# Optimization experiments

Measured on AMD Instinct MI355X. Metric: run time of the kernel, lower is better.

The kernel has to match this reference:

```python
import jax, jax.numpy as jnp
import numpy as np

# Mamba2 defaults (mamba_ssm): expand=2, headdim=64, d_conv=4, ngroups=1
D_MODEL, D_STATE, D_INNER, HEADDIM, D_CONV = 512, 64, 1024, 64, 4
NHEADS = D_INNER // HEADDIM  # 16
CONV_DIM = D_INNER + 2 * D_STATE  # 1152
D_IN_PROJ = 2 * D_INNER + 2 * D_STATE + NHEADS  # 2192
BATCH, SEQLEN = 2, 2048
RMS_EPS = 1.1920929e-07  # torch nn.RMSNorm eps=None -> fp32 machine eps
GNORM_EPS = 1e-5  # mamba_ssm RMSNormGated default


def _rms(t, w, eps):
    return t * jax.lax.rsqrt(jnp.mean(t * t, axis=-1, keepdims=True) + eps) * w


def _mamba2(u, in_w, conv_w, conv_b, dt_bias, A_log, Dp, gnorm_w, out_w):
    """Mamba2 block forward (ngroups=1). u: (b, l, d_model) -> (b, l, d_model)."""
    b, l, _ = u.shape
    zxbcdt = jnp.einsum('bld,ed->ble', u, in_w)  # (b, l, 2192)
    z = zxbcdt[..., :D_INNER]
    xBC = zxbcdt[..., D_INNER:D_INNER + CONV_DIM]
    dt = jax.nn.softplus(zxbcdt[..., -NHEADS:] + dt_bias)  # (b, l, h)
    # causal depthwise conv, kernel D_CONV, then SiLU
    xp = jnp.pad(xBC, ((0, 0), (D_CONV - 1, 0), (0, 0)))
    xBC = conv_b + sum(xp[:, i:i + l, :] * conv_w[:, i] for i in range(D_CONV))
    xBC = jax.nn.silu(xBC)
    x = xBC[..., :D_INNER].reshape(b, l, NHEADS, HEADDIM)
    Bm = xBC[..., D_INNER:D_INNER + D_STATE]  # (b, l, n)
    Cm = xBC[..., D_INNER + D_STATE:]         # (b, l, n)
    dA = jnp.exp(dt * (-jnp.exp(A_log)))      # (b, l, h), decay per head

    def step(h, inp):
        dA_t, dt_t, B_t, C_t, x_t = inp  # (b,h) (b,h) (b,n) (b,n) (b,h,p)
        h = h * dA_t[:, :, None, None] + jnp.einsum('bh,bhp,bn->bhpn', dt_t, x_t, B_t)
        y = jnp.einsum('bhpn,bn->bhp', h, C_t)
        return h, y

    h0 = jnp.zeros((b, NHEADS, HEADDIM, D_STATE), u.dtype)
    xs = (jnp.swapaxes(dA, 0, 1), jnp.swapaxes(dt, 0, 1), jnp.swapaxes(Bm, 0, 1),
          jnp.swapaxes(Cm, 0, 1), jnp.swapaxes(x, 0, 1))
    _, ys = jax.lax.scan(step, h0, xs)  # (l, b, h, p)
    y = jnp.swapaxes(ys, 0, 1) + x * Dp[None, None, :, None]
    y = y.reshape(b, l, D_INNER)
    # gated RMSNorm: norm(y * silu(z)) * weight
    y = y * jax.nn.silu(z)
    y = _rms(y, gnorm_w, GNORM_EPS)
    return jnp.einsum('bli,oi->blo', y, out_w)


def _layer(x, pos_emb, pixel_mask, norm_ssm_w, norm_ffn_w, ffn_w1, ffn_b1, ffn_w2, ffn_b2,
           f_in_w, f_conv_w, f_conv_b, f_dt_bias, f_A_log, f_D, f_gnorm_w, f_out_w,
           b_in_w, b_conv_w, b_conv_b, b_dt_bias, b_A_log, b_D, b_gnorm_w, b_out_w):
    si = _rms(x, norm_ssm_w, RMS_EPS) + pos_emb
    fwd = _mamba2(si, f_in_w, f_conv_w, f_conv_b, f_dt_bias, f_A_log, f_D, f_gnorm_w, f_out_w)
    bwd = jnp.flip(_mamba2(jnp.flip(si, 1), b_in_w, b_conv_w, b_conv_b, b_dt_bias,
                           b_A_log, b_D, b_gnorm_w, b_out_w), 1)
    ssm_out = (fwd + bwd) * pixel_mask[..., None]  # merge='add'
    x = x + ssm_out
    h = _rms(x, norm_ffn_w, RMS_EPS)
    h = jax.nn.gelu(h @ ffn_w1.T + ffn_b1, approximate=False)
    return x + (h @ ffn_w2.T + ffn_b2)


def setup_inputs() -> dict:
    key = jax.random.key(0)
    ks = jax.random.split(key, 16)
    f32 = jnp.float32
    inp = {}
    inp['x'] = jax.random.normal(ks[0], (BATCH, SEQLEN, D_MODEL), f32)
    inp['pos_emb'] = jax.random.normal(ks[1], (BATCH, SEQLEN, D_MODEL), f32) * 0.02
    inp['pixel_mask'] = jnp.ones((BATCH, SEQLEN), f32)
    inp['norm_ssm_w'] = jnp.ones((D_MODEL,), f32)
    inp['norm_ffn_w'] = jnp.ones((D_MODEL,), f32)
    d_ffn = 4 * D_MODEL
    inp['ffn_w1'] = jax.random.normal(ks[2], (d_ffn, D_MODEL), f32) * 0.02
    inp['ffn_b1'] = jnp.zeros((d_ffn,), f32)
    inp['ffn_w2'] = jax.random.normal(ks[3], (D_MODEL, d_ffn), f32) * 0.02
    inp['ffn_b2'] = jnp.zeros((D_MODEL,), f32)
    i = 4
    for pre in ('f', 'b'):
        inp[pre + '_in_w'] = jax.random.normal(ks[i], (D_IN_PROJ, D_MODEL), f32) * 0.02; i += 1
        inp[pre + '_conv_w'] = jax.random.uniform(ks[i], (CONV_DIM, D_CONV), f32, -0.5, 0.5); i += 1
        inp[pre + '_conv_b'] = jnp.zeros((CONV_DIM,), f32)
        dt0 = jnp.exp(jax.random.uniform(ks[i], (NHEADS,), f32) * (jnp.log(0.1) - jnp.log(0.001)) + jnp.log(0.001)); i += 1
        inp[pre + '_dt_bias'] = dt0 + jnp.log(-jnp.expm1(-dt0))  # inverse softplus
        inp[pre + '_A_log'] = jnp.log(jax.random.uniform(ks[i], (NHEADS,), f32, 1.0, 16.0)); i += 1
        inp[pre + '_D'] = jnp.ones((NHEADS,), f32)
        inp[pre + '_gnorm_w'] = jnp.ones((D_INNER,), f32)
        inp[pre + '_out_w'] = jax.random.normal(ks[i], (D_MODEL, D_INNER), f32) * 0.02; i += 1
    return inp


def reference(x, pos_emb, pixel_mask, norm_ssm_w, norm_ffn_w, ffn_w1, ffn_b1, ffn_w2, ffn_b2,
              f_in_w, f_conv_w, f_conv_b, f_dt_bias, f_A_log, f_D, f_gnorm_w, f_out_w,
              b_in_w, b_conv_w, b_conv_b, b_dt_bias, b_A_log, b_D, b_gnorm_w, b_out_w):
    return _layer(x, pos_emb, pixel_mask, norm_ssm_w, norm_ffn_w, ffn_w1, ffn_b1, ffn_w2, ffn_b2,
                  f_in_w, f_conv_w, f_conv_b, f_dt_bias, f_A_log, f_D, f_gnorm_w, f_out_w,
                  b_in_w, b_conv_w, b_conv_b, b_dt_bias, b_A_log, b_D, b_gnorm_w, b_out_w)
```

## Files before the change

### kernel.cpp

```cpp
#include <hip/hip_runtime.h>
#include <hip/hip_bf16.h>

typedef unsigned short u16;
typedef unsigned int u32;
typedef __bf16 bf16x8 __attribute__((ext_vector_type(8)));
typedef float f32x4 __attribute__((ext_vector_type(4)));

typedef __attribute__((address_space(1))) void gvoid_t;
typedef __attribute__((address_space(3))) void lvoid_t;
__device__ __forceinline__ void lds_cp16(void* lds, const void* g) {
    __builtin_amdgcn_global_load_lds((gvoid_t*)g, (lvoid_t*)lds, 16, 0, 0);
}

__device__ __forceinline__ float bf2f(u16 v) {
    u32 x = (u32)v << 16;
    return __builtin_bit_cast(float, x);
}
__device__ __forceinline__ u16 f2bf(float f) {
    return __builtin_bit_cast(u16, (__bf16)f);
}

__device__ __forceinline__ float block_sum_256(float v, float* red) {
    #pragma unroll
    for (int o = 32; o > 0; o >>= 1) v += __shfl_xor(v, o);
    int w = threadIdx.x >> 6;
    if ((threadIdx.x & 63) == 0) red[w] = v;
    __syncthreads();
    return red[0] + red[1] + red[2] + red[3];
}

__global__ __launch_bounds__(256) void k_prep(
    const float* __restrict__ f_inw, const float* __restrict__ b_inw,
    const float* __restrict__ f_ow, const float* __restrict__ b_ow,
    const float* __restrict__ w1, const float* __restrict__ w2,
    u16* __restrict__ INWF, u16* __restrict__ INWB,
    u16* __restrict__ OWF, u16* __restrict__ OWB,
    u16* __restrict__ W1B, u16* __restrict__ W2B,
    const float* __restrict__ x, const float* __restrict__ pe,
    const float* __restrict__ wrms, u16* __restrict__ sib) {
    if (blockIdx.x < 21504) {
        int i = blockIdx.x * 256 + threadIdx.x;
        if (i < 1179648) { int n = i >> 9; INWF[i] = (n < 2192) ? f2bf(f_inw[i]) : (u16)0; return; }
        i -= 1179648;
        if (i < 1179648) { int n = i >> 9; INWB[i] = (n < 2192) ? f2bf(b_inw[i]) : (u16)0; return; }
        i -= 1179648;
        if (i < 524288) { OWF[i] = f2bf(f_ow[i]); return; }
        i -= 524288;
        if (i < 524288) { OWB[i] = f2bf(b_ow[i]); return; }
        i -= 524288;
        if (i < 1048576) { W1B[i] = f2bf(w1[i]); return; }
        i -= 1048576;
        if (i < 1048576) W2B[i] = f2bf(w2[i]);
        return;
    }
    __shared__ float red[4];
    int row = blockIdx.x - 21504, t = threadIdx.x;
    size_t base = (size_t)row * 512 + t * 2;
    float2 xv = *(const float2*)(x + base);
    float ss = block_sum_256(xv.x * xv.x + xv.y * xv.y, red);
    float sc = rsqrtf(ss * (1.f / 512.f) + 1.1920929e-07f);
    float2 pv = *(const float2*)(pe + base);
    float2 wv = *(const float2*)(wrms + t * 2);
    sib[base] = f2bf(xv.x * sc * wv.x + pv.x);
    sib[base + 1] = f2bf(xv.y * sc * wv.y + pv.y);
}

__global__ __launch_bounds__(256) void k_gemm_in(
    const u16* __restrict__ A, const u16* __restrict__ W0, const u16* __restrict__ W1,
    u16* __restrict__ Z0, u16* __restrict__ Z1,
    u16* __restrict__ XB0, u16* __restrict__ XB1) {
    const int z = blockIdx.z;
    const u16* W = z ? W1 : W0;
    u16* Z = z ? Z1 : Z0;
    u16* XB = z ? XB1 : XB0;
    const int K = 512;

    __shared__ __align__(16) u16 As[128 * 32];
    __shared__ __align__(16) u16 Bs[128 * 32];

    const int t = threadIdx.x;
    const int lane = t & 63;
    const int w = t >> 6;
    const int m0 = blockIdx.y * 128;
    const int n0 = blockIdx.x * 128;
    const int wm = (w >> 1) * 64;
    const int wn = (w & 1) * 64;
    const int fr = lane & 15;
    const int fk = (lane >> 4) * 8;

    f32x4 acc[4][4];
    #pragma unroll
    for (int i = 0; i < 4; ++i)
        #pragma unroll
        for (int j = 0; j < 4; ++j) acc[i][j] = (f32x4){0.f, 0.f, 0.f, 0.f};

    for (int kt = 0; kt < K; kt += 32) {
        #pragma unroll
        for (int j = 0; j < 2; ++j) {
            int off16 = j * 256 + t;
            int row = off16 >> 2;
            int kc = (off16 & 3) * 8;
            int gm = m0 + row;
            if (z) gm = (gm & ~2047) | (2047 - (gm & 2047));
            lds_cp16(As + off16 * 8, A + (size_t)gm * K + kt + kc);
            lds_cp16(Bs + off16 * 8, W + (size_t)(n0 + row) * K + kt + kc);
        }
        __syncthreads();
        bf16x8 af[4], bfr[4];
        #pragma unroll
        for (int i = 0; i < 4; ++i) af[i] = *(const bf16x8*)(As + (wm + i * 16 + fr) * 32 + fk);
        #pragma unroll
        for (int i = 0; i < 4; ++i) bfr[i] = *(const bf16x8*)(Bs + (wn + i * 16 + fr) * 32 + fk);
        #pragma unroll
        for (int i = 0; i < 4; ++i)
            #pragma unroll
            for (int j = 0; j < 4; ++j)
                acc[i][j] = __builtin_amdgcn_mfma_f32_16x16x32_bf16(af[i], bfr[j], acc[i][j], 0, 0, 0);
        __syncthreads();
    }
    #pragma unroll
    for (int i = 0; i < 4; ++i) {
        int rbase = m0 + wm + i * 16 + (lane >> 4) * 4;
        #pragma unroll
        for (int j = 0; j < 4; ++j) {
            int c = n0 + wn + j * 16 + fr;
            #pragma unroll
            for (int r = 0; r < 4; ++r) {
                u16 v = f2bf(acc[i][j][r]);
                int m = rbase + r;
                if (c < 1024) Z[(size_t)m * 1024 + c] = v;
                else if (c < 2192) XB[(size_t)m * 1184 + (c - 1024)] = v;
            }
        }
    }
}

template <int EPI>
__global__ __launch_bounds__(256) void k_gemm128(
    const u16* __restrict__ A0, const u16* __restrict__ A1,
    const u16* __restrict__ W0, const u16* __restrict__ W1,
    u16* __restrict__ C0, u16* __restrict__ C1, int N, int K,
    const float* __restrict__ bias, const float* __restrict__ resid,
    float* __restrict__ outf) {
    const int z = blockIdx.z;
    const u16* A = z ? A1 : A0;
    const u16* W = z ? W1 : W0;
    u16* C = z ? C1 : C0;

    __shared__ __align__(16) u16 As[128 * 32];
    __shared__ __align__(16) u16 Bs[128 * 32];

    const int t = threadIdx.x;
    const int lane = t & 63;
    const int w = t >> 6;
    const int m0 = blockIdx.y * 128;
    const int n0 = blockIdx.x * 128;
    const int wm = (w >> 1) * 64;
    const int wn = (w & 1) * 64;
    const int fr = lane & 15;
    const int fk = (lane >> 4) * 8;

    f32x4 acc[4][4];
    #pragma unroll
    for (int i = 0; i < 4; ++i)
        #pragma unroll
        for (int j = 0; j < 4; ++j) acc[i][j] = (f32x4){0.f, 0.f, 0.f, 0.f};

    for (int kt = 0; kt < K; kt += 32) {
        #pragma unroll
        for (int j = 0; j < 2; ++j) {
            int off16 = j * 256 + t;
            int row = off16 >> 2;
            int kc = (off16 & 3) * 8;
            lds_cp16(As + off16 * 8, A + (size_t)(m0 + row) * K + kt + kc);
            lds_cp16(Bs + off16 * 8, W + (size_t)(n0 + row) * K + kt + kc);
        }
        __syncthreads();
        bf16x8 af[4], bfr[4];
        #pragma unroll
        for (int i = 0; i < 4; ++i) af[i] = *(const bf16x8*)(As + (wm + i * 16 + fr) * 32 + fk);
        #pragma unroll
        for (int i = 0; i < 4; ++i) bfr[i] = *(const bf16x8*)(Bs + (wn + i * 16 + fr) * 32 + fk);
        #pragma unroll
        for (int i = 0; i < 4; ++i)
            #pragma unroll
            for (int j = 0; j < 4; ++j)
                acc[i][j] = __builtin_amdgcn_mfma_f32_16x16x32_bf16(af[i], bfr[j], acc[i][j], 0, 0, 0);
        __syncthreads();
    }
    #pragma unroll
    for (int i = 0; i < 4; ++i) {
        int rbase = m0 + wm + i * 16 + (lane >> 4) * 4;
        #pragma unroll
        for (int j = 0; j < 4; ++j) {
            int col = n0 + wn + j * 16 + fr;
            #pragma unroll
            for (int r = 0; r < 4; ++r) {
                int m = rbase + r;
                float v = acc[i][j][r];
                if (EPI == 0) {
                    C[(size_t)m * N + col] = f2bf(v);
                } else if (EPI == 1) {
                    float xg = v + bias[col];
                    C[(size_t)m * N + col] = f2bf(0.5f * xg * (1.f + erff(xg * 0.70710678118654752f)));
                } else {
                    outf[(size_t)m * N + col] = v + bias[col] + resid[(size_t)m * N + col];
                }
            }
        }
    }
}

template <int EPI>
__global__ __launch_bounds__(256) void k_gemm12864(
    const u16* __restrict__ A0, const u16* __restrict__ A1,
    const u16* __restrict__ W0, const u16* __restrict__ W1,
    u16* __restrict__ C0, u16* __restrict__ C1, int N, int K,
    const float* __restrict__ bias, const float* __restrict__ resid,
    float* __restrict__ outf) {
    const int z = blockIdx.z;
    const u16* A = z ? A1 : A0;
    const u16* W = z ? W1 : W0;
    u16* C = z ? C1 : C0;

    __shared__ __align__(16) u16 As[128 * 32];
    __shared__ __align__(16) u16 Bs[64 * 32];

    const int t = threadIdx.x;
    const int lane = t & 63;
    const int w = t >> 6;
    const int m0 = blockIdx.y * 128;
    const int n0 = blockIdx.x * 64;
    const int wm = w * 32;
    const int fr = lane & 15;
    const int fk = (lane >> 4) * 8;

    f32x4 acc[2][4];
    #pragma unroll
    for (int i = 0; i < 2; ++i)
        #pragma unroll
        for (int j = 0; j < 4; ++j) acc[i][j] = (f32x4){0.f, 0.f, 0.f, 0.f};

    for (int kt = 0; kt < K; kt += 32) {
        #pragma unroll
        for (int j = 0; j < 2; ++j) {
            int off16 = j * 256 + t;
            int row = off16 >> 2;
            int kc = (off16 & 3) * 8;
            lds_cp16(As + off16 * 8, A + (size_t)(m0 + row) * K + kt + kc);
        }
        lds_cp16(Bs + t * 8, W + (size_t)(n0 + (t >> 2)) * K + kt + (t & 3) * 8);
        __syncthreads();
        bf16x8 af[2], bfr[4];
        #pragma unroll
        for (int i = 0; i < 2; ++i) af[i] = *(const bf16x8*)(As + (wm + i * 16 + fr) * 32 + fk);
        #pragma unroll
        for (int j = 0; j < 4; ++j) bfr[j] = *(const bf16x8*)(Bs + (j * 16 + fr) * 32 + fk);
        #pragma unroll
        for (int i = 0; i < 2; ++i)
            #pragma unroll
            for (int j = 0; j < 4; ++j)
                acc[i][j] = __builtin_amdgcn_mfma_f32_16x16x32_bf16(af[i], bfr[j], acc[i][j], 0, 0, 0);
        __syncthreads();
    }
    #pragma unroll
    for (int i = 0; i < 2; ++i) {
        int rbase = m0 + wm + i * 16 + (lane >> 4) * 4;
        #pragma unroll
        for (int j = 0; j < 4; ++j) {
            int col = n0 + j * 16 + fr;
            #pragma unroll
            for (int r = 0; r < 4; ++r) {
                int m = rbase + r;
                float v = acc[i][j][r];
                if (EPI == 0) {
                    C[(size_t)m * N + col] = f2bf(v);
                } else if (EPI == 1) {
                    float xg = v + bias[col];
                    C[(size_t)m * N + col] = f2bf(0.5f * xg * (1.f + erff(xg * 0.70710678118654752f)));
                } else {
                    outf[(size_t)m * N + col] = v + bias[col] + resid[(size_t)m * N + col];
                }
            }
        }
    }
}

__global__ __launch_bounds__(160) void k_conv(
    const u16* __restrict__ xb0, const u16* __restrict__ xb1,
    const float* __restrict__ cw0, const float* __restrict__ cb0,
    const float* __restrict__ dtb0, const float* __restrict__ al0,
    const float* __restrict__ cw1, const float* __restrict__ cb1,
    const float* __restrict__ dtb1, const float* __restrict__ al1,
    u16* __restrict__ xc0, u16* __restrict__ xc1,
    float* __restrict__ dtO0, float* __restrict__ dAO0,
    float* __restrict__ dtO1, float* __restrict__ dAO1) {
    int g = blockIdx.x;
    int dir = g >> 9;
    int row0 = (g & 511) * 8;
    const u16* xb = dir ? xb1 : xb0;
    const float* cw = dir ? cw1 : cw0;
    const float* cb = dir ? cb1 : cb0;
    const float* dtb = dir ? dtb1 : dtb0;
    const float* al = dir ? al1 : al0;
    u16* xc = dir ? xc1 : xc0;
    float* dtO = dir ? dtO1 : dtO0;
    float* dAO = dir ? dAO1 : dAO0;
    int tl0 = row0 & 2047;
    int rbatch = row0 - tl0;
    int t = threadIdx.x;
    if (t < 144) {
        int col = t * 8;
        float cwa[8][4];
        #pragma unroll
        for (int j = 0; j < 8; ++j) {
            float4 c4 = *(const float4*)(cw + (col + j) * 4);
            cwa[j][0] = c4.x; cwa[j][1] = c4.y; cwa[j][2] = c4.z; cwa[j][3] = c4.w;
        }
        float cbv[8];
        float4 cb0v = *(const float4*)(cb + col);
        float4 cb1v = *(const float4*)(cb + col + 4);
        cbv[0] = cb0v.x; cbv[1] = cb0v.y; cbv[2] = cb0v.z; cbv[3] = cb0v.w;
        cbv[4] = cb1v.x; cbv[5] = cb1v.y; cbv[6] = cb1v.z; cbv[7] = cb1v.w;
        uint4 win[4];
        win[0] = win[1] = win[2] = make_uint4(0, 0, 0, 0);
        #pragma unroll
        for (int i = 0; i < 3; ++i) {
            int tt = tl0 - 3 + i;
            if (tt >= 0) win[i] = *(const uint4*)(xb + (size_t)(rbatch + tt) * 1184 + col);
        }
        for (int s = 0; s < 8; ++s) {
            win[3] = *(const uint4*)(xb + (size_t)(rbatch + tl0 + s) * 1184 + col);
            const u16* w0 = (const u16*)&win[0];
            const u16* w1 = (const u16*)&win[1];
            const u16* w2 = (const u16*)&win[2];
            const u16* w3 = (const u16*)&win[3];
            u16 ov[8];
            #pragma unroll
            for (int j = 0; j < 8; ++j) {
                float a = cbv[j] + bf2f(w0[j]) * cwa[j][0] + bf2f(w1[j]) * cwa[j][1]
                        + bf2f(w2[j]) * cwa[j][2] + bf2f(w3[j]) * cwa[j][3];
                ov[j] = f2bf(a / (1.f + expf(-a)));
            }
            *(uint4*)(xc + (size_t)(row0 + s) * 1152 + col) = *(const uint4*)ov;
            win[0] = win[1]; win[1] = win[2]; win[2] = win[3];
        }
    } else if (t < 160) {
        int hh = t - 144;
        float nal = -expf(al[hh]);
        float dtbv = dtb[hh];
        for (int s = 0; s < 8; ++s) {
            int row = row0 + s;
            float v = bf2f(xb[(size_t)row * 1184 + 1152 + hh]) + dtbv;
            float sp = (v > 20.f) ? v : log1pf(expf(v));
            dtO[row * 16 + hh] = sp;
            dAO[row * 16 + hh] = nal * sp;
        }
    }
}

__global__ __launch_bounds__(256) void k_ssd_state(
    const u16* __restrict__ xc0, const float* __restrict__ dt0, const float* __restrict__ ld0,
    const u16* __restrict__ xc1, const float* __restrict__ dt1, const float* __restrict__ ld1,
    float* __restrict__ S, float* __restrict__ Aprod) {
    int blk = blockIdx.x;
    int c = blk & 31, h = (blk >> 5) & 15, b = (blk >> 9) & 1, dir = blk >> 10;
    const u16* xc = dir ? xc1 : xc0;
    const float* dtp = dir ? dt1 : dt0;
    const float* ldp = dir ? ld1 : ld0;
    const int t = threadIdx.x, w = t >> 6, lane = t & 63;
    const int fr = lane & 15, fk = (lane >> 4) * 8;

    __shared__ __align__(16) u16 sBt[64 * 72];
    __shared__ __align__(16) u16 sXp[64 * 72];
    __shared__ float ssc[64];
    size_t row0 = (size_t)b * 2048 + c * 64;

    if (t < 64) {
        float v = ldp[(row0 + t) * 16 + h];
        float dtv = dtp[(row0 + t) * 16 + h];
        #pragma unroll
        for (int o = 1; o < 64; o <<= 1) {
            float u = __shfl_up(v, o);
            if (lane >= o) v += u;
        }
        float last = __shfl(v, 63);
        ssc[t] = dtv * expf(last - v);
        if (t == 63) Aprod[blk] = expf(v);
    }
    __syncthreads();
    #pragma unroll
    for (int i2 = t; i2 < 512; i2 += 256) {
        int r = i2 >> 3, e8 = (i2 & 7) * 8;
        size_t rb = (row0 + r) * 1152;
        uint4 bv = *(const uint4*)(xc + rb + 1024 + e8);
        uint4 xv = *(const uint4*)(xc + rb + h * 64 + e8);
        const u16* bs = (const u16*)&bv;
        const u16* xs = (const u16*)&xv;
        float sc = ssc[r];
        #pragma unroll
        for (int j = 0; j < 8; ++j) {
            sBt[(e8 + j) * 72 + r] = bs[j];
            sXp[(e8 + j) * 72 + r] = f2bf(bf2f(xs[j]) * sc);
        }
    }
    __syncthreads();

    f32x4 acc[4];
    #pragma unroll
    for (int j = 0; j < 4; ++j) acc[j] = (f32x4){0.f, 0.f, 0.f, 0.f};
    #pragma unroll
    for (int k0 = 0; k0 < 64; k0 += 32) {
        bf16x8 a = *(const bf16x8*)(sBt + (w * 16 + fr) * 72 + k0 + fk);
        #pragma unroll
        for (int j = 0; j < 4; ++j) {
            bf16x8 bb = *(const bf16x8*)(sXp + (j * 16 + fr) * 72 + k0 + fk);
            acc[j] = __builtin_amdgcn_mfma_f32_16x16x32_bf16(a, bb, acc[j], 0, 0, 0);
        }
    }
    float* Sb = S + (size_t)blk * 4096;
    int nb = w * 16 + (lane >> 4) * 4;
    #pragma unroll
    for (int j = 0; j < 4; ++j) {
        int p = j * 16 + fr;
        *(f32x4*)(Sb + p * 64 + nb) = acc[j];
    }
}

__global__ __launch_bounds__(256) void k_scan_carry(float* __restrict__ S,
                                                    const float* __restrict__ Aprod) {
    int g = blockIdx.x;
    int blk = g >> 4;
    int e = (g & 15) * 256 + threadIdx.x;
    size_t base = (size_t)blk * 32 * 4096 + e;
    float sv[32];
    #pragma unroll
    for (int c = 0; c < 32; ++c) sv[c] = S[base + (size_t)c * 4096];
    float ap[32];
    #pragma unroll
    for (int c = 0; c < 32; ++c) ap[c] = Aprod[blk * 32 + c];
    float h = 0.f;
    #pragma unroll
    for (int c = 0; c < 32; ++c) {
        S[base + (size_t)c * 4096] = h;
        h = ap[c] * h + sv[c];
    }
}

__global__ __launch_bounds__(256) void k_ssd_y(
    const u16* __restrict__ xc0, const float* __restrict__ dt0, const float* __restrict__ ld0,
    const float* __restrict__ Dv0, u16* __restrict__ y0,
    const u16* __restrict__ xc1, const float* __restrict__ dt1, const float* __restrict__ ld1,
    const float* __restrict__ Dv1, u16* __restrict__ y1,
    const float* __restrict__ S) {
    int blk = blockIdx.x;
    int c = blk & 31, h = (blk >> 5) & 15, b = (blk >> 9) & 1, dir = blk >> 10;
    const u16* xc = dir ? xc1 : xc0;
    const float* dtp = dir ? dt1 : dt0;
    const float* ldp = dir ? ld1 : ld0;
    u16* y = dir ? y1 : y0;
    const float Dh = (dir ? Dv1 : Dv0)[h];
    const int t = threadIdx.x, w = t >> 6, lane = t & 63;
    const int fr = lane & 15, fk = (lane >> 4) * 8;

    __shared__ __align__(16) u16 sB[64 * 72];
    __shared__ __align__(16) u16 sC[64 * 72];
    __shared__ __align__(16) u16 sXp[64 * 72];
    __shared__ __align__(16) u16 sHi[64 * 72];
    __shared__ __align__(16) u16 sLo[64 * 72];
    __shared__ __align__(16) u16 sGl[64 * 72];
    __shared__ float scl[64], sdt[64];
    size_t row0 = (size_t)b * 2048 + c * 64;

    if (t < 64) {
        float v = ldp[(row0 + t) * 16 + h];
        float dtv = dtp[(row0 + t) * 16 + h];
        #pragma unroll
        for (int o = 1; o < 64; o <<= 1) {
            float u = __shfl_up(v, o);
            if (lane >= o) v += u;
        }
        scl[t] = v;
        sdt[t] = dtv;
    }
    __syncthreads();
    #pragma unroll
    for (int i2 = t; i2 < 512; i2 += 256) {
        int r = i2 >> 3, e8 = (i2 & 7) * 8;
        size_t rb = (row0 + r) * 1152;
        *(uint4*)(sB + r * 72 + e8) = *(const uint4*)(xc + rb + 1024 + e8);
        *(uint4*)(sC + r * 72 + e8) = *(const uint4*)(xc + rb + 1088 + e8);
        uint4 xv = *(const uint4*)(xc + rb + h * 64 + e8);
        const u16* xs = (const u16*)&xv;
        float dtv = sdt[r];
        #pragma unroll
        for (int j = 0; j < 8; ++j) sXp[(e8 + j) * 72 + r] = f2bf(bf2f(xs[j]) * dtv);
    }
    #pragma unroll
    for (int i4 = t; i4 < 1024; i4 += 256) {
        int p = i4 >> 4, n4 = (i4 & 15) * 4;
        float4 hv = *(const float4*)(S + (size_t)blk * 4096 + p * 64 + n4);
        ushort4 hi4, lo4;
        hi4.x = f2bf(hv.x); lo4.x = f2bf(hv.x - bf2f(hi4.x));
        hi4.y = f2bf(hv.y); lo4.y = f2bf(hv.y - bf2f(hi4.y));
        hi4.z = f2bf(hv.z); lo4.z = f2bf(hv.z - bf2f(hi4.z));
        hi4.w = f2bf(hv.w); lo4.w = f2bf(hv.w - bf2f(hi4.w));
        *(ushort4*)(sHi + p * 72 + n4) = hi4;
        *(ushort4*)(sLo + p * 72 + n4) = lo4;
    }
    __syncthreads();

    f32x4 g[4], acc2[4];
    #pragma unroll
    for (int j = 0; j < 4; ++j) { g[j] = (f32x4){0.f,0.f,0.f,0.f}; acc2[j] = (f32x4){0.f,0.f,0.f,0.f}; }
    #pragma unroll
    for (int k0 = 0; k0 < 64; k0 += 32) {
        bf16x8 a = *(const bf16x8*)(sC + (w * 16 + fr) * 72 + k0 + fk);
        #pragma unroll
        for (int j = 0; j < 4; ++j) {
            bf16x8 bb = *(const bf16x8*)(sB + (j * 16 + fr) * 72 + k0 + fk);
            g[j] = __builtin_amdgcn_mfma_f32_16x16x32_bf16(a, bb, g[j], 0, 0, 0);
            bf16x8 bh = *(const bf16x8*)(sHi + (j * 16 + fr) * 72 + k0 + fk);
            acc2[j] = __builtin_amdgcn_mfma_f32_16x16x32_bf16(a, bh, acc2[j], 0, 0, 0);
            bf16x8 bl = *(const bf16x8*)(sLo + (j * 16 + fr) * 72 + k0 + fk);
            acc2[j] = __builtin_amdgcn_mfma_f32_16x16x32_bf16(a, bl, acc2[j], 0, 0, 0);
        }
    }
    #pragma unroll
    for (int j = 0; j < 4; ++j) {
        int r = j * 16 + fr;
        #pragma unroll
        for (int reg = 0; reg < 4; ++reg) {
            int s = w * 16 + (lane >> 4) * 4 + reg;
            float val = (r <= s) ? expf(scl[s] - scl[r]) * g[j][reg] : 0.f;
            sGl[s * 72 + r] = f2bf(val);
        }
    }
    __syncthreads();

    f32x4 acc1[4];
    #pragma unroll
    for (int j = 0; j < 4; ++j) acc1[j] = (f32x4){0.f, 0.f, 0.f, 0.f};
    #pragma unroll
    for (int k0 = 0; k0 < 64; k0 += 32) {
        bf16x8 a = *(const bf16x8*)(sGl + (w * 16 + fr) * 72 + k0 + fk);
        #pragma unroll
        for (int j = 0; j < 4; ++j) {
            bf16x8 bb = *(const bf16x8*)(sXp + (j * 16 + fr) * 72 + k0 + fk);
            acc1[j] = __builtin_amdgcn_mfma_f32_16x16x32_bf16(a, bb, acc1[j], 0, 0, 0);
        }
    }
    #pragma unroll
    for (int reg = 0; reg < 4; ++reg) {
        int s = w * 16 + (lane >> 4) * 4 + reg;
        float es = expf(scl[s]);
        size_t yrb = (row0 + s) * 1024 + h * 64;
        size_t xrb = (row0 + s) * 1152 + h * 64;
        #pragma unroll
        for (int j = 0; j < 4; ++j) {
            int p = j * 16 + fr;
            float xv = bf2f(xc[xrb + p]);
            y[yrb + p] = f2bf(acc1[j][reg] + es * acc2[j][reg] + xv * Dh);
        }
    }
}

__global__ __launch_bounds__(256) void k_gnorm(
    const u16* __restrict__ y0, const u16* __restrict__ z0,
    const float* __restrict__ gw0, u16* __restrict__ o0,
    const u16* __restrict__ y1, const u16* __restrict__ z1,
    const float* __restrict__ gw1, u16* __restrict__ o1) {
    __shared__ float red[4];
    int r = blockIdx.x;
    int dir = r >> 12, row = r & 4095;
    int t = threadIdx.x;
    const u16* y = dir ? y1 : y0;
    const u16* zp = dir ? z1 : z0;
    const float* gw = dir ? gw1 : gw0;
    u16* o = dir ? o1 : o0;
    ushort4 yv = *(const ushort4*)(y + (size_t)row * 1024 + t * 4);
    ushort4 zr = *(const ushort4*)(zp + (size_t)row * 1024 + t * 4);
    float z0f = bf2f(zr.x), z1f = bf2f(zr.y), z2f = bf2f(zr.z), z3f = bf2f(zr.w);
    float v0 = bf2f(yv.x) * (z0f / (1.f + expf(-z0f)));
    float v1 = bf2f(yv.y) * (z1f / (1.f + expf(-z1f)));
    float v2 = bf2f(yv.z) * (z2f / (1.f + expf(-z2f)));
    float v3 = bf2f(yv.w) * (z3f / (1.f + expf(-z3f)));
    float ss = block_sum_256(v0 * v0 + v1 * v1 + v2 * v2 + v3 * v3, red);
    float sc = rsqrtf(ss * (1.f / 1024.f) + 1e-5f);
    float4 gv = *(const float4*)(gw + t * 4);
    size_t ob = (size_t)row * 1024 + t * 4;
    o[ob + 0] = f2bf(v0 * sc * gv.x);
    o[ob + 1] = f2bf(v1 * sc * gv.y);
    o[ob + 2] = f2bf(v2 * sc * gv.z);
    o[ob + 3] = f2bf(v3 * sc * gv.w);
}

__global__ __launch_bounds__(256) void k_add_rms(
    const float* __restrict__ x, const u16* __restrict__ of,
    const u16* __restrict__ ob, const float* __restrict__ mask,
    const float* __restrict__ wrms,
    float* __restrict__ x2, u16* __restrict__ o) {
    __shared__ float red[4];
    int row = blockIdx.x, t = threadIdx.x;
    int bb = row >> 11, tl = row & 2047;
    size_t fb = (size_t)((bb << 11) + (2047 - tl)) * 512;
    float m = mask[row];
    size_t base = (size_t)row * 512 + t * 2;
    size_t fo = fb + t * 2;
    float2 xv = *(const float2*)(x + base);
    float v0 = xv.x + (bf2f(of[base]) + bf2f(ob[fo])) * m;
    float v1 = xv.y + (bf2f(of[base + 1]) + bf2f(ob[fo + 1])) * m;
    x2[base] = v0;
    x2[base + 1] = v1;
    float ss = block_sum_256(v0 * v0 + v1 * v1, red);
    float sc = rsqrtf(ss * (1.f / 512.f) + 1.1920929e-07f);
    float2 wv = *(const float2*)(wrms + t * 2);
    o[base] = f2bf(v0 * sc * wv.x);
    o[base + 1] = f2bf(v1 * sc * wv.y);
}

extern "C" void kernel_launch(void* const* d_in, const int* in_sizes, int n_in,
                              void* d_out, int out_size, void* d_ws, size_t ws_size,
                              hipStream_t stream) {
    const float* x = (const float*)d_in[0];
    const float* pe = (const float*)d_in[1];
    const float* mask = (const float*)d_in[2];
    const float* nsw = (const float*)d_in[3];
    const float* nfw = (const float*)d_in[4];
    const float* w1 = (const float*)d_in[5];
    const float* b1 = (const float*)d_in[6];
    const float* w2 = (const float*)d_in[7];
    const float* b2 = (const float*)d_in[8];
    const float* f_inw = (const float*)d_in[9];
    const float* f_cw = (const float*)d_in[10];
    const float* f_cb = (const float*)d_in[11];
    const float* f_dtb = (const float*)d_in[12];
    const float* f_al = (const float*)d_in[13];
    const float* f_D = (const float*)d_in[14];
    const float* f_gw = (const float*)d_in[15];
    const float* f_ow = (const float*)d_in[16];
    const float* b_inw = (const float*)d_in[17];
    const float* b_cw = (const float*)d_in[18];
    const float* b_cb = (const float*)d_in[19];
    const float* b_dtb = (const float*)d_in[20];
    const float* b_al = (const float*)d_in[21];
    const float* b_D = (const float*)d_in[22];
    const float* b_gw = (const float*)d_in[23];
    const float* b_ow = (const float*)d_in[24];
    float* out = (float*)d_out;

    char* ws = (char*)d_ws;
    u16* Z0   = (u16*)(ws + 0);
    u16* Z1   = (u16*)(ws + 8388608);
    u16* XB0  = (u16*)(ws + 16777216);
    u16* XB1  = (u16*)(ws + 26476544);
    u16* INWF = (u16*)(ws + 36175872);
    u16* INWB = (u16*)(ws + 38535168);
    u16* SIB  = (u16*)(ws + 40894464);
    u16* XC0  = (u16*)(ws + 36175872);
    u16* XC1  = (u16*)(ws + 45613056);
    float* dtF = (float*)(ws + 55050240);
    float* dAF = (float*)(ws + 55312384);
    float* dtB = (float*)(ws + 55574528);
    float* dAB = (float*)(ws + 55836672);
    u16* Y0   = (u16*)(ws + 16777216);
    u16* Y1   = (u16*)(ws + 25165824);
    u16* YG0  = (u16*)(ws + 36175872);
    u16* YG1  = (u16*)(ws + 44564480);
    u16* OP0  = (u16*)(ws + 0);
    u16* OP1  = (u16*)(ws + 4194304);
    float* X2 = (float*)(ws + 8388608);
    u16* X2B  = (u16*)(ws + 0);
    u16* HACT = (u16*)(ws + 16777216);
    u16* OWF = (u16*)(ws + 56098816);
    u16* OWB = (u16*)(ws + 57147392);
    u16* W1B = (u16*)(ws + 58195968);
    u16* W2B = (u16*)(ws + 60293120);
    float* SBUF = (float*)(ws + 62390272);
    float* APR  = (float*)(ws + 95944704);

    k_prep<<<25600, 256, 0, stream>>>(f_inw, b_inw, f_ow, b_ow, w1, w2,
                                      INWF, INWB, OWF, OWB, W1B, W2B,
                                      x, pe, nsw, SIB);
    k_gemm_in<<<dim3(18, 32, 2), 256, 0, stream>>>(SIB, INWF, INWB, Z0, Z1, XB0, XB1);
    k_conv<<<1024, 160, 0, stream>>>(XB0, XB1, f_cw, f_cb, f_dtb, f_al,
                                     b_cw, b_cb, b_dtb, b_al,
                                     XC0, XC1, dtF, dAF, dtB, dAB);
    k_ssd_state<<<2048, 256, 0, stream>>>(XC0, dtF, dAF, XC1, dtB, dAB, SBUF, APR);
    k_scan_carry<<<1024, 256, 0, stream>>>(SBUF, APR);
    k_ssd_y<<<2048, 256, 0, stream>>>(XC0, dtF, dAF, f_D, Y0,
                                      XC1, dtB, dAB, b_D, Y1, SBUF);
    k_gnorm<<<8192, 256, 0, stream>>>(Y0, Z0, f_gw, YG0, Y1, Z1, b_gw, YG1);
    k_gemm12864<0><<<dim3(8, 32, 2), 256, 0, stream>>>(YG0, YG1, OWF, OWB, OP0, OP1, 512, 1024,
                                                       nullptr, nullptr, nullptr);
    k_add_rms<<<4096, 256, 0, stream>>>(x, OP0, OP1, mask, nfw, X2, X2B);
    k_gemm128<1><<<dim3(16, 32, 1), 256, 0, stream>>>(X2B, X2B, W1B, W1B, HACT, HACT, 2048, 512,
                                                      b1, nullptr, nullptr);
    k_gemm12864<2><<<dim3(8, 32, 1), 256, 0, stream>>>(HACT, HACT, W2B, W2B, nullptr, nullptr,
                                                       512, 2048, b2, X2, out);
}
```

Measured before the change: 342.6 us.

## Double-buffer LDS tiles in all GEMMs and use 64x64 tiles for FFN down-proj

Every GEMM kernel now keeps two LDS buffers and issues the async global-to-LDS copies for the next K-slice before running the MFMAs on the current one, so loads overlap compute and one barrier per iteration is dropped. A new 64x64-tile GEMM kernel replaces the 128x64 kernel for the FFN down projection (K=2048, N=512), doubling the block count to improve occupancy across CUs. The trade-offs are twice the LDS per block, which may lower occupancy, and less reuse per tile in the smaller kernel.

```diff
diff --git a/kernel.cpp b/kernel.cpp
--- a/kernel.cpp
+++ b/kernel.cpp
@@ -75,8 +75,8 @@
     u16* XB = z ? XB1 : XB0;
     const int K = 512;
 
-    __shared__ __align__(16) u16 As[128 * 32];
-    __shared__ __align__(16) u16 Bs[128 * 32];
+    __shared__ __align__(16) u16 As[2][128 * 32];
+    __shared__ __align__(16) u16 Bs[2][128 * 32];
 
     const int t = threadIdx.x;
     const int lane = t & 63;
@@ -94,7 +94,7 @@
         #pragma unroll
         for (int j = 0; j < 4; ++j) acc[i][j] = (f32x4){0.f, 0.f, 0.f, 0.f};
 
-    for (int kt = 0; kt < K; kt += 32) {
+    auto STAGE = [&](int buf, int kt) {
         #pragma unroll
         for (int j = 0; j < 2; ++j) {
             int off16 = j * 256 + t;
@@ -102,21 +102,28 @@
             int kc = (off16 & 3) * 8;
             int gm = m0 + row;
             if (z) gm = (gm & ~2047) | (2047 - (gm & 2047));
-            lds_cp16(As + off16 * 8, A + (size_t)gm * K + kt + kc);
-            lds_cp16(Bs + off16 * 8, W + (size_t)(n0 + row) * K + kt + kc);
-        }
-        __syncthreads();
+            lds_cp16(As[buf] + off16 * 8, A + (size_t)gm * K + kt + kc);
+            lds_cp16(Bs[buf] + off16 * 8, W + (size_t)(n0 + row) * K + kt + kc);
+        }
+    };
+
+    STAGE(0, 0);
+    __syncthreads();
+    int cur = 0;
+    for (int kt = 0; kt < K; kt += 32) {
+        if (kt + 32 < K) STAGE(cur ^ 1, kt + 32);
         bf16x8 af[4], bfr[4];
         #pragma unroll
-        for (int i = 0; i < 4; ++i) af[i] = *(const bf16x8*)(As + (wm + i * 16 + fr) * 32 + fk);
-        #pragma unroll
-        for (int i = 0; i < 4; ++i) bfr[i] = *(const bf16x8*)(Bs + (wn + i * 16 + fr) * 32 + fk);
+        for (int i = 0; i < 4; ++i) af[i] = *(const bf16x8*)(As[cur] + (wm + i * 16 + fr) * 32 + fk);
+        #pragma unroll
+        for (int i = 0; i < 4; ++i) bfr[i] = *(const bf16x8*)(Bs[cur] + (wn + i * 16 + fr) * 32 + fk);
         #pragma unroll
         for (int i = 0; i < 4; ++i)
             #pragma unroll
             for (int j = 0; j < 4; ++j)
                 acc[i][j] = __builtin_amdgcn_mfma_f32_16x16x32_bf16(af[i], bfr[j], acc[i][j], 0, 0, 0);
         __syncthreads();
+        cur ^= 1;
     }
     #pragma unroll
     for (int i = 0; i < 4; ++i) {
@@ -147,8 +154,8 @@
     const u16* W = z ? W1 : W0;
     u16* C = z ? C1 : C0;
 
-    __shared__ __align__(16) u16 As[128 * 32];
-    __shared__ __align__(16) u16 Bs[128 * 32];
+    __shared__ __align__(16) u16 As[2][128 * 32];
+    __shared__ __align__(16) u16 Bs[2][128 * 32];
 
     const int t = threadIdx.x;
     const int lane = t & 63;
@@ -166,27 +173,34 @@
         #pragma unroll
         for (int j = 0; j < 4; ++j) acc[i][j] = (f32x4){0.f, 0.f, 0.f, 0.f};
 
-    for (int kt = 0; kt < K; kt += 32) {
+    auto STAGE = [&](int buf, int kt) {
         #pragma unroll
         for (int j = 0; j < 2; ++j) {
             int off16 = j * 256 + t;
             int row = off16 >> 2;
             int kc = (off16 & 3) * 8;
-            lds_cp16(As + off16 * 8, A + (size_t)(m0 + row) * K + kt + kc);
-            lds_cp16(Bs + off16 * 8, W + (size_t)(n0 + row) * K + kt + kc);
-        }
-        __syncthreads();
+            lds_cp16(As[buf] + off16 * 8, A + (size_t)(m0 + row) * K + kt + kc);
+            lds_cp16(Bs[buf] + off16 * 8, W + (size_t)(n0 + row) * K + kt + kc);
+        }
+    };
+
+    STAGE(0, 0);
+    __syncthreads();
+    int cur = 0;
+    for (int kt = 0; kt < K; kt += 32) {
+        if (kt + 32 < K) STAGE(cur ^ 1, kt + 32);
         bf16x8 af[4], bfr[4];
         #pragma unroll
-        for (int i = 0; i < 4; ++i) af[i] = *(const bf16x8*)(As + (wm + i * 16 + fr) * 32 + fk);
-        #pragma unroll
-        for (int i = 0; i < 4; ++i) bfr[i] = *(const bf16x8*)(Bs + (wn + i * 16 + fr) * 32 + fk);
+        for (int i = 0; i < 4; ++i) af[i] = *(const bf16x8*)(As[cur] + (wm + i * 16 + fr) * 32 + fk);
+        #pragma unroll
+        for (int i = 0; i < 4; ++i) bfr[i] = *(const bf16x8*)(Bs[cur] + (wn + i * 16 + fr) * 32 + fk);
         #pragma unroll
         for (int i = 0; i < 4; ++i)
             #pragma unroll
             for (int j = 0; j < 4; ++j)
                 acc[i][j] = __builtin_amdgcn_mfma_f32_16x16x32_bf16(af[i], bfr[j], acc[i][j], 0, 0, 0);
         __syncthreads();
+        cur ^= 1;
     }
     #pragma unroll
     for (int i = 0; i < 4; ++i) {
@@ -223,8 +237,8 @@
     const u16* W = z ? W1 : W0;
     u16* C = z ? C1 : C0;
 
-    __shared__ __align__(16) u16 As[128 * 32];
-    __shared__ __align__(16) u16 Bs[64 * 32];
+    __shared__ __align__(16) u16 As[2][128 * 32];
+    __shared__ __align__(16) u16 Bs[2][64 * 32];
 
     const int t = threadIdx.x;
     const int lane = t & 63;
@@ -241,27 +255,34 @@
         #pragma unroll
         for (int j = 0; j < 4; ++j) acc[i][j] = (f32x4){0.f, 0.f, 0.f, 0.f};
 
-    for (int kt = 0; kt < K; kt += 32) {
+    auto STAGE = [&](int buf, int kt) {
         #pragma unroll
         for (int j = 0; j < 2; ++j) {
             int off16 = j * 256 + t;
             int row = off16 >> 2;
             int kc = (off16 & 3) * 8;
-            lds_cp16(As + off16 * 8, A + (size_t)(m0 + row) * K + kt + kc);
-        }
-        lds_cp16(Bs + t * 8, W + (size_t)(n0 + (t >> 2)) * K + kt + (t & 3) * 8);
-        __syncthreads();
+            lds_cp16(As[buf] + off16 * 8, A + (size_t)(m0 + row) * K + kt + kc);
+        }
+        lds_cp16(Bs[buf] + t * 8, W + (size_t)(n0 + (t >> 2)) * K + kt + (t & 3) * 8);
+    };
+
+    STAGE(0, 0);
+    __syncthreads();
+    int cur = 0;
+    for (int kt = 0; kt < K; kt += 32) {
+        if (kt + 32 < K) STAGE(cur ^ 1, kt + 32);
         bf16x8 af[2], bfr[4];
         #pragma unroll
-        for (int i = 0; i < 2; ++i) af[i] = *(const bf16x8*)(As + (wm + i * 16 + fr) * 32 + fk);
-        #pragma unroll
-        for (int j = 0; j < 4; ++j) bfr[j] = *(const bf16x8*)(Bs + (j * 16 + fr) * 32 + fk);
+        for (int i = 0; i < 2; ++i) af[i] = *(const bf16x8*)(As[cur] + (wm + i * 16 + fr) * 32 + fk);
+        #pragma unroll
+        for (int j = 0; j < 4; ++j) bfr[j] = *(const bf16x8*)(Bs[cur] + (j * 16 + fr) * 32 + fk);
         #pragma unroll
         for (int i = 0; i < 2; ++i)
             #pragma unroll
             for (int j = 0; j < 4; ++j)
                 acc[i][j] = __builtin_amdgcn_mfma_f32_16x16x32_bf16(af[i], bfr[j], acc[i][j], 0, 0, 0);
         __syncthreads();
+        cur ^= 1;
     }
     #pragma unroll
     for (int i = 0; i < 2; ++i) {
@@ -269,6 +290,85 @@
         #pragma unroll
         for (int j = 0; j < 4; ++j) {
             int col = n0 + j * 16 + fr;
+            #pragma unroll
+            for (int r = 0; r < 4; ++r) {
+                int m = rbase + r;
+                float v = acc[i][j][r];
+                if (EPI == 0) {
+                    C[(size_t)m * N + col] = f2bf(v);
+                } else if (EPI == 1) {
+                    float xg = v + bias[col];
+                    C[(size_t)m * N + col] = f2bf(0.5f * xg * (1.f + erff(xg * 0.70710678118654752f)));
+                } else {
+                    outf[(size_t)m * N + col] = v + bias[col] + resid[(size_t)m * N + col];
+                }
+            }
+        }
+    }
+}
+
+template <int EPI>
+__global__ __launch_bounds__(256) void k_gemm64(
+    const u16* __restrict__ A0, const u16* __restrict__ A1,
+    const u16* __restrict__ W0, const u16* __restrict__ W1,
+    u16* __restrict__ C0, u16* __restrict__ C1, int N, int K,
+    const float* __restrict__ bias, const float* __restrict__ resid,
+    float* __restrict__ outf) {
+    const int z = blockIdx.z;
+    const u16* A = z ? A1 : A0;
+    const u16* W = z ? W1 : W0;
+    u16* C = z ? C1 : C0;
+
+    __shared__ __align__(16) u16 As[2][64 * 32];
+    __shared__ __align__(16) u16 Bs[2][64 * 32];
+
+    const int t = threadIdx.x;
+    const int lane = t & 63;
+    const int w = t >> 6;
+    const int m0 = blockIdx.y * 64;
+    const int n0 = blockIdx.x * 64;
+    const int wm = (w >> 1) * 32;
+    const int wn = (w & 1) * 32;
+    const int fr = lane & 15;
+    const int fk = (lane >> 4) * 8;
+
+    f32x4 acc[2][2];
+    #pragma unroll
+    for (int i = 0; i < 2; ++i)
+        #pragma unroll
+        for (int j = 0; j < 2; ++j) acc[i][j] = (f32x4){0.f, 0.f, 0.f, 0.f};
+
+    const int srow = t >> 2;
+    const int skc = (t & 3) * 8;
+    auto STAGE = [&](int buf, int kt) {
+        lds_cp16(As[buf] + t * 8, A + (size_t)(m0 + srow) * K + kt + skc);
+        lds_cp16(Bs[buf] + t * 8, W + (size_t)(n0 + srow) * K + kt + skc);
+    };
+
+    STAGE(0, 0);
+    __syncthreads();
+    int cur = 0;
+    for (int kt = 0; kt < K; kt += 32) {
+        if (kt + 32 < K) STAGE(cur ^ 1, kt + 32);
+        bf16x8 af[2], bfr[2];
+        #pragma unroll
+        for (int i = 0; i < 2; ++i) af[i] = *(const bf16x8*)(As[cur] + (wm + i * 16 + fr) * 32 + fk);
+        #pragma unroll
+        for (int j = 0; j < 2; ++j) bfr[j] = *(const bf16x8*)(Bs[cur] + (wn + j * 16 + fr) * 32 + fk);
+        #pragma unroll
+        for (int i = 0; i < 2; ++i)
+            #pragma unroll
+            for (int j = 0; j < 2; ++j)
+                acc[i][j] = __builtin_amdgcn_mfma_f32_16x16x32_bf16(af[i], bfr[j], acc[i][j], 0, 0, 0);
+        __syncthreads();
+        cur ^= 1;
+    }
+    #pragma unroll
+    for (int i = 0; i < 2; ++i) {
+        int rbase = m0 + wm + i * 16 + (lane >> 4) * 4;
+        #pragma unroll
+        for (int j = 0; j < 2; ++j) {
+            int col = n0 + wn + j * 16 + fr;
             #pragma unroll
             for (int r = 0; r < 4; ++r) {
                 int m = rbase + r;
@@ -696,6 +796,6 @@
     k_add_rms<<<4096, 256, 0, stream>>>(x, OP0, OP1, mask, nfw, X2, X2B);
     k_gemm128<1><<<dim3(16, 32, 1), 256, 0, stream>>>(X2B, X2B, W1B, W1B, HACT, HACT, 2048, 512,
                                                       b1, nullptr, nullptr);
-    k_gemm12864<2><<<dim3(8, 32, 1), 256, 0, stream>>>(HACT, HACT, W2B, W2B, nullptr, nullptr,
-                                                       512, 2048, b2, X2, out);
-}
+    k_gemm64<2><<<dim3(8, 64, 1), 256, 0, stream>>>(HACT, HACT, W2B, W2B, nullptr, nullptr,
+                                                    512, 2048, b2, X2, out);
+}
```

Result: faster. 335.6 us (-2.0%).
